# Optimization experiments

Measured on AMD Instinct MI355X. Metric: run time of the kernel, lower is better.

## Reference

```python
import jax, jax.numpy as jnp
import numpy as np

N_NODES = 50000
E_RAW = 1600000
EMB_DIM = 32
HID = 128
OUT = 128


def setup_inputs() -> dict:
    key = jax.random.key(0)
    k1, k2, k3, k4, k5, k6 = jax.random.split(key, 6)
    x = jnp.arange(N_NODES, dtype=jnp.int64)
    edge_index = jax.random.randint(k1, (2, E_RAW), 0, N_NODES, dtype=jnp.int64)
    emb = jax.random.normal(k2, (N_NODES, EMB_DIM), dtype=jnp.float32)
    W1 = jax.random.normal(k3, (EMB_DIM, HID), dtype=jnp.float32) / np.sqrt(EMB_DIM)
    b1 = jnp.zeros((HID,), dtype=jnp.float32)
    W2 = jax.random.normal(k4, (HID, OUT), dtype=jnp.float32) / np.sqrt(HID)
    b2 = jnp.zeros((OUT,), dtype=jnp.float32)
    return {"x": x, "edge_index": edge_index, "emb": emb,
            "W1": W1, "b1": b1, "W2": W2, "b2": b2}


def _gcn_norm(edge_index, num_nodes):
    # add self-loops, then symmetric normalization deg^-1/2 A_hat deg^-1/2
    loop = jnp.arange(num_nodes, dtype=edge_index.dtype)
    src = jnp.concatenate([edge_index[0], loop])
    dst = jnp.concatenate([edge_index[1], loop])
    ones = jnp.ones(src.shape[0], dtype=jnp.float32)
    deg = jax.ops.segment_sum(ones, dst, num_segments=num_nodes)
    dinv = jax.lax.rsqrt(deg)  # deg >= 1 due to self-loops
    norm = dinv[src] * dinv[dst]  # [E+N]
    return src, dst, norm


def _gcn_conv(h, src, dst, norm, W, b, num_nodes):
    h = h @ W                                  # [N, d_out] dense GEMM
    msg = h[src] * norm[:, None]               # gather + edge scale
    agg = jax.ops.segment_sum(msg, dst, num_segments=num_nodes)  # scatter-add
    return agg + b


def reference(x, edge_index, emb, W1, b1, W2, b2):
    num_nodes = emb.shape[0]
    h = emb[x]                                 # embedding lookup
    src, dst, norm = _gcn_norm(edge_index, num_nodes)
    h = _gcn_conv(h, src, dst, norm, W1, b1, num_nodes)
    h = jax.nn.relu(h)
    out = _gcn_conv(h, src, dst, norm, W2, b2, num_nodes)
    return out
```

## Files before the change

kernel.cpp:

```cpp
#include <hip/hip_runtime.h>


#define NPP   6250
#define NC    32

typedef float vfloat4 __attribute__((ext_vector_type(4)));

static inline int cdiv(int a, int b){ return (a + b - 1) / b; }

__device__ __forceinline__ unsigned short f2bf(float f){
    unsigned int u = __float_as_uint(f);
    u += 0x7fffu + ((u >> 16) & 1u);
    return (unsigned short)(u >> 16);
}
__device__ __forceinline__ float bf2f(unsigned short b){
    return __uint_as_float(((unsigned int)b) << 16);
}

__device__ __forceinline__ void nt_store4(float* p, const float4& v){
    vfloat4 t = {v.x, v.y, v.z, v.w};
    __builtin_nontemporal_store(t, (vfloat4*)p);
}

__global__ void k_zero_i32(int* __restrict__ p, int n){
    int i = blockIdx.x * blockDim.x + threadIdx.x;
    if (i < n) p[i] = 0;
}

__global__ __launch_bounds__(256) void k_bucket(const int* __restrict__ src,
        const int* __restrict__ dst, int E, int* __restrict__ staged,
        int* __restrict__ gcur, int npp, int C){
    __shared__ int qcnt[8];
    __shared__ int qbase[8];
    __shared__ int qbuf[8 * 256];
    int tid = threadIdx.x;
    if (tid < 8) qcnt[tid] = 0;
    __syncthreads();
    int e0 = blockIdx.x * 1024 + tid * 4;
    if (e0 + 3 < E){
        int4 d4 = *(const int4*)(dst + e0);
        int4 s4 = *(const int4*)(src + e0);
        int dd[4] = {d4.x, d4.y, d4.z, d4.w};
        int ss[4] = {s4.x, s4.y, s4.z, s4.w};
        #pragma unroll
        for (int i = 0; i < 4; i++){
            int p = dd[i] / npp;
            int pk = ((dd[i] - p * npp) << 17) | ss[i];
            int pos = atomicAdd(&qcnt[p], 1);
            if (pos < 256) qbuf[p * 256 + pos] = pk;
            else {
                int gp = atomicAdd(&gcur[p], 1);
                staged[(size_t)p * C + gp] = pk;
            }
        }
    } else {
        for (int e = e0; e < E && e < e0 + 4; e++){
            int d = dst[e], s = src[e];
            int p = d / npp;
            int pk = ((d - p * npp) << 17) | s;
            int pos = atomicAdd(&qcnt[p], 1);
            if (pos < 256) qbuf[p * 256 + pos] = pk;
            else {
                int gp = atomicAdd(&gcur[p], 1);
                staged[(size_t)p * C + gp] = pk;
            }
        }
    }
    __syncthreads();
    if (tid < 8){
        int nq = min(qcnt[tid], 256);
        qbase[tid] = (nq > 0) ? atomicAdd(&gcur[tid], nq) : 0;
    }
    __syncthreads();
    for (int b = 0; b < 8; b++){
        int nq = min(qcnt[b], 256);
        int gb = qbase[b];
        for (int i = tid; i < nq; i += 256)
            staged[(size_t)b * C + gb + i] = qbuf[b * 256 + i];
    }
}

__global__ __launch_bounds__(256) void k_hist(const int* __restrict__ staged,
        const int* __restrict__ gcur, int C, int CH, int npp, int* __restrict__ H){
    __shared__ int hist[NPP];
    int part  = blockIdx.x & 7;
    int chunk = blockIdx.x >> 3;
    int tid = threadIdx.x;
    for (int i = tid; i < npp; i += 256) hist[i] = 0;
    __syncthreads();
    int pc = gcur[part];
    int e0 = chunk * CH, e1 = min(e0 + CH, pc);
    const int* sd = staged + (size_t)part * C;
    for (int e = e0 + tid; e < e1; e += 256)
        atomicAdd(&hist[(unsigned)sd[e] >> 17], 1);
    __syncthreads();
    int* Hrow = H + (size_t)(part * NC + chunk) * npp;
    for (int i = tid; i < npp; i += 256) Hrow[i] = hist[i];
}

__global__ __launch_bounds__(256) void k_nodescan(int* __restrict__ H, int npp, int n,
        int* __restrict__ ecount, float* __restrict__ dinv, int* __restrict__ bsum){
    __shared__ int s[256];
    int t = blockIdx.x * 256 + threadIdx.x;
    int run = 0;
    if (t < 8 * npp && t < n){
        int p  = t / npp;
        int dl = t - p * npp;
        #pragma unroll
        for (int c = 0; c < NC; c++){
            size_t idx = (size_t)(p * NC + c) * npp + dl;
            int v = H[idx];
            H[idx] = run;
            run += v;
        }
        ecount[t] = run;
        dinv[t] = rsqrtf((float)run + 1.0f);
    }
    s[threadIdx.x] = run;
    __syncthreads();
    for (int d = 128; d > 0; d >>= 1){
        if (threadIdx.x < d) s[threadIdx.x] += s[threadIdx.x + d];
        __syncthreads();
    }
    if (threadIdx.x == 0) bsum[blockIdx.x] = s[0];
}

__global__ __launch_bounds__(256) void k_scanBC(const int* __restrict__ ecount, int n,
        const int* __restrict__ bsum, int nb, int* __restrict__ offsets){
    __shared__ int bs[256];
    __shared__ int s[256];
    int t = threadIdx.x;
    bs[t] = (t < nb) ? bsum[t] : 0;
    __syncthreads();
    if (t == 0){
        int run = 0;
        for (int b = 0; b < nb; b++){ int v = bs[b]; bs[b] = run; run += v; }
    }
    __syncthreads();
    int i = blockIdx.x * 256 + t;
    int v = (i < n) ? ecount[i] : 0;
    s[t] = v;
    __syncthreads();
    for (int d = 1; d < 256; d <<= 1){
        int x = (t >= d) ? s[t - d] : 0;
        __syncthreads();
        s[t] += x;
        __syncthreads();
    }
    if (i < n) offsets[i] = bs[blockIdx.x] + s[t] - v;
}

__global__ __launch_bounds__(256) void k_fill3(const int* __restrict__ staged,
        const int* __restrict__ gcur, int C, int CH, int npp,
        const int* __restrict__ H, const int* __restrict__ offsets,
        int* __restrict__ csr_src){
    __shared__ int cur[NPP];
    int part  = blockIdx.x & 7;
    int chunk = blockIdx.x >> 3;
    int tid = threadIdx.x;
    const int* Hrow = H + (size_t)(part * NC + chunk) * npp;
    for (int i = tid; i < npp; i += 256) cur[i] = Hrow[i];
    __syncthreads();
    int pc = gcur[part];
    int lo = part * npp;
    int e0 = chunk * CH, e1 = min(e0 + CH, pc);
    const int* sd = staged + (size_t)part * C;
    for (int e = e0 + tid; e < e1; e += 256){
        int pk = sd[e];
        int dl = (unsigned)pk >> 17;
        int r = atomicAdd(&cur[dl], 1);
        csr_src[offsets[lo + dl] + r] = pk & 0x1FFFF;
    }
}

__global__ void k_scale(const float* __restrict__ emb, const int* __restrict__ x,
                        const float* __restrict__ dinv, unsigned short* __restrict__ es, int n){
    int idx = blockIdx.x * blockDim.x + threadIdx.x;
    if (idx >= n * 32) return;
    int i = idx >> 5;
    int c = idx & 31;
    es[idx] = f2bf(emb[(size_t)x[i] * 32 + c] * dinv[i]);
}

__global__ __launch_bounds__(256) void k_l1(const unsigned short* __restrict__ es,
        const int* __restrict__ offsets, const int* __restrict__ ecount,
        const int* __restrict__ csr, const float* __restrict__ dinv,
        const float* __restrict__ W1, const float* __restrict__ b1,
        unsigned short* __restrict__ hs, int n){
    __shared__ float w[32 * 128];
    __shared__ float a1t[8][32];
    for (int i = threadIdx.x; i < 32 * 128; i += 256) w[i] = W1[i];
    int g    = threadIdx.x >> 5;
    int lane = threadIdx.x & 31;
    int node = blockIdx.x * 8 + g;
    if (node < n){
        int off = offsets[node], cnt = ecount[node];
        float s0 = bf2f(es[(size_t)node * 32 + lane]);
        float s1 = 0.f;
        int e = 0;
        for (; e + 16 <= cnt; e += 16){
            int idx[16];
            #pragma unroll
            for (int i = 0; i < 16; i++) idx[i] = csr[off + e + i];
            unsigned short v[16];
            #pragma unroll
            for (int i = 0; i < 16; i++) v[i] = es[(size_t)idx[i] * 32 + lane];
            #pragma unroll
            for (int i = 0; i < 16; i += 2){
                s0 += bf2f(v[i]);
                s1 += bf2f(v[i + 1]);
            }
        }
        for (; e + 8 <= cnt; e += 8){
            int idx[8];
            #pragma unroll
            for (int i = 0; i < 8; i++) idx[i] = csr[off + e + i];
            unsigned short v[8];
            #pragma unroll
            for (int i = 0; i < 8; i++) v[i] = es[(size_t)idx[i] * 32 + lane];
            #pragma unroll
            for (int i = 0; i < 8; i += 2){
                s0 += bf2f(v[i]);
                s1 += bf2f(v[i + 1]);
            }
        }
        for (; e < cnt; e++) s0 += bf2f(es[(size_t)csr[off + e] * 32 + lane]);
        a1t[g][lane] = dinv[node] * (s0 + s1);
    }
    __syncthreads();
    if (node >= n) return;
    int c4 = lane * 4;
    float4 acc = *(const float4*)(b1 + c4);
    #pragma unroll
    for (int k4 = 0; k4 < 8; k4++){
        float4 av = *(const float4*)&a1t[g][k4 * 4];
        float4 w0 = *(const float4*)&w[(k4 * 4 + 0) * 128 + c4];
        float4 w1 = *(const float4*)&w[(k4 * 4 + 1) * 128 + c4];
        float4 w2 = *(const float4*)&w[(k4 * 4 + 2) * 128 + c4];
        float4 w3 = *(const float4*)&w[(k4 * 4 + 3) * 128 + c4];
        acc.x += av.x * w0.x + av.y * w1.x + av.z * w2.x + av.w * w3.x;
        acc.y += av.x * w0.y + av.y * w1.y + av.z * w2.y + av.w * w3.y;
        acc.z += av.x * w0.z + av.y * w1.z + av.z * w2.z + av.w * w3.z;
        acc.w += av.x * w0.w + av.y * w1.w + av.z * w2.w + av.w * w3.w;
    }
    float dv = dinv[node];
    ushort4 o;
    o.x = f2bf(dv * fmaxf(acc.x, 0.f));
    o.y = f2bf(dv * fmaxf(acc.y, 0.f));
    o.z = f2bf(dv * fmaxf(acc.z, 0.f));
    o.w = f2bf(dv * fmaxf(acc.w, 0.f));
    *(ushort4*)(hs + (size_t)node * 128 + c4) = o;
}

__global__ __launch_bounds__(256, 5) void k_l2(const unsigned short* __restrict__ hs,
        const int* __restrict__ offsets, const int* __restrict__ ecount,
        const int* __restrict__ csr, const float* __restrict__ dinv,
        const float* __restrict__ W2, const float* __restrict__ b2,
        float* __restrict__ out, int n){
    __shared__ float a2t[32 * 128];
    int g    = threadIdx.x >> 5;
    int lane = threadIdx.x & 31;
    int c4g  = lane * 4;
    #pragma unroll
    for (int j = 0; j < 4; j++){
        int nl = g + 8 * j;
        int node = blockIdx.x * 32 + nl;
        if (node < n){
            int off = offsets[node], cnt = ecount[node];
            ushort4 sv = *(const ushort4*)(hs + (size_t)node * 128 + c4g);
            float ax0 = bf2f(sv.x), ax1 = 0.f;
            float ay0 = bf2f(sv.y), ay1 = 0.f;
            float az0 = bf2f(sv.z), az1 = 0.f;
            float aw0 = bf2f(sv.w), aw1 = 0.f;
            int e = 0;
            for (; e + 16 <= cnt; e += 16){
                int idx[16];
                #pragma unroll
                for (int i = 0; i < 16; i++) idx[i] = csr[off + e + i];
                ushort4 v[16];
                #pragma unroll
                for (int i = 0; i < 16; i++)
                    v[i] = *(const ushort4*)(hs + (size_t)idx[i] * 128 + c4g);
                #pragma unroll
                for (int i = 0; i < 16; i += 2){
                    ax0 += bf2f(v[i].x); ax1 += bf2f(v[i + 1].x);
                    ay0 += bf2f(v[i].y); ay1 += bf2f(v[i + 1].y);
                    az0 += bf2f(v[i].z); az1 += bf2f(v[i + 1].z);
                    aw0 += bf2f(v[i].w); aw1 += bf2f(v[i + 1].w);
                }
            }
            for (; e + 8 <= cnt; e += 8){
                int idx[8];
                #pragma unroll
                for (int i = 0; i < 8; i++) idx[i] = csr[off + e + i];
                ushort4 v[8];
                #pragma unroll
                for (int i = 0; i < 8; i++)
                    v[i] = *(const ushort4*)(hs + (size_t)idx[i] * 128 + c4g);
                #pragma unroll
                for (int i = 0; i < 8; i += 2){
                    ax0 += bf2f(v[i].x); ax1 += bf2f(v[i + 1].x);
                    ay0 += bf2f(v[i].y); ay1 += bf2f(v[i + 1].y);
                    az0 += bf2f(v[i].z); az1 += bf2f(v[i + 1].z);
                    aw0 += bf2f(v[i].w); aw1 += bf2f(v[i + 1].w);
                }
            }
            for (; e < cnt; e++){
                ushort4 v = *(const ushort4*)(hs + (size_t)csr[off + e] * 128 + c4g);
                ax0 += bf2f(v.x); ay0 += bf2f(v.y); az0 += bf2f(v.z); aw0 += bf2f(v.w);
            }
            float dv = dinv[node];
            float4 r;
            r.x = dv * (ax0 + ax1); r.y = dv * (ay0 + ay1);
            r.z = dv * (az0 + az1); r.w = dv * (aw0 + aw1);
            *(float4*)&a2t[nl * 128 + c4g] = r;
        }
    }
    __syncthreads();
    int c4 = lane * 4;
    int r0 = (threadIdx.x >> 5) * 4;
    float4 bias = *(const float4*)(b2 + c4);
    float4 acc0 = bias, acc1 = bias, acc2 = bias, acc3 = bias;
    for (int k = 0; k < 128; k += 4){
        float4 a0  = *(const float4*)&a2t[(r0 + 0) * 128 + k];
        float4 a1v = *(const float4*)&a2t[(r0 + 1) * 128 + k];
        float4 a2v = *(const float4*)&a2t[(r0 + 2) * 128 + k];
        float4 a3v = *(const float4*)&a2t[(r0 + 3) * 128 + k];
        #pragma unroll
        for (int kk = 0; kk < 4; kk++){
            float4 wv = *(const float4*)(W2 + (size_t)(k + kk) * 128 + c4);
            float b0 = (kk == 0) ? a0.x  : (kk == 1) ? a0.y  : (kk == 2) ? a0.z  : a0.w;
            float b1v= (kk == 0) ? a1v.x : (kk == 1) ? a1v.y : (kk == 2) ? a1v.z : a1v.w;
            float b2v= (kk == 0) ? a2v.x : (kk == 1) ? a2v.y : (kk == 2) ? a2v.z : a2v.w;
            float b3 = (kk == 0) ? a3v.x : (kk == 1) ? a3v.y : (kk == 2) ? a3v.z : a3v.w;
            acc0.x += b0 * wv.x; acc0.y += b0 * wv.y; acc0.z += b0 * wv.z; acc0.w += b0 * wv.w;
            acc1.x += b1v * wv.x; acc1.y += b1v * wv.y; acc1.z += b1v * wv.z; acc1.w += b1v * wv.w;
            acc2.x += b2v * wv.x; acc2.y += b2v * wv.y; acc2.z += b2v * wv.z; acc2.w += b2v * wv.w;
            acc3.x += b3 * wv.x; acc3.y += b3 * wv.y; acc3.z += b3 * wv.z; acc3.w += b3 * wv.w;
        }
    }
    int rb = blockIdx.x * 32 + r0;
    if (rb + 0 < n) nt_store4(out + (size_t)(rb + 0) * 128 + c4, acc0);
    if (rb + 1 < n) nt_store4(out + (size_t)(rb + 1) * 128 + c4, acc1);
    if (rb + 2 < n) nt_store4(out + (size_t)(rb + 2) * 128 + c4, acc2);
    if (rb + 3 < n) nt_store4(out + (size_t)(rb + 3) * 128 + c4, acc3);
}

extern "C" void kernel_launch(void* const* d_in, const int* in_sizes, int n_in,
                              void* d_out, int out_size, void* d_ws, size_t ws_size,
                              hipStream_t stream){
    const int*   x    = (const int*)d_in[0];
    const int*   ei   = (const int*)d_in[1];
    const float* emb  = (const float*)d_in[2];
    const float* W1   = (const float*)d_in[3];
    const float* b1   = (const float*)d_in[4];
    const float* W2   = (const float*)d_in[5];
    const float* b2   = (const float*)d_in[6];
    const int N = in_sizes[0];
    const int E = in_sizes[1] / 2;
    const int* srcv = ei;
    const int* dstv = ei + E;
    float* out = (float*)d_out;

    char* p = (char*)d_ws;
    auto alloc = [&](size_t bytes) -> char* {
        char* r = p; p += (bytes + 255) & ~(size_t)255; return r;
    };
    int nb = cdiv(N, 256);
    int*            ecount  = (int*)           alloc((size_t)(N + 8) * 4);
    int*            gcur    = ecount + N;
    int*            offsets = (int*)           alloc((size_t)N * 4);
    int*            bsum    = (int*)           alloc((size_t)nb * 4);
    float*          dinv    = (float*)         alloc((size_t)N * 4);
    int*            csr     = (int*)           alloc((size_t)E * 4);
    unsigned short* es      = (unsigned short*)alloc((size_t)N * 32 * 2);
    int*            H       = (int*)           alloc((size_t)8 * NC * NPP * 4);
    unsigned short* hs      = (unsigned short*)alloc((size_t)N * 128 * 2);
    int*            staged  = (int*)           alloc((size_t)(E + 8 * 65536) * 4);
    (void)ws_size; (void)n_in; (void)out_size;

    const int npp = cdiv(N, 8);
    const int C   = E / 8 + 65536;
    const int CH  = cdiv(C, NC);

    k_zero_i32<<<1, 64, 0, stream>>>(gcur, 8);
    k_bucket  <<<cdiv(E, 1024), 256, 0, stream>>>(srcv, dstv, E, staged, gcur, npp, C);
    k_hist    <<<8 * NC, 256, 0, stream>>>(staged, gcur, C, CH, npp, H);
    k_nodescan<<<nb, 256, 0, stream>>>(H, npp, N, ecount, dinv, bsum);
    k_scanBC  <<<nb, 256, 0, stream>>>(ecount, N, bsum, nb, offsets);
    k_fill3   <<<8 * NC, 256, 0, stream>>>(staged, gcur, C, CH, npp, H, offsets, csr);

    k_scale <<<cdiv(N * 32, 256), 256, 0, stream>>>(emb, x, dinv, es, N);
    k_l1    <<<cdiv(N, 8), 256, 0, stream>>>(es, offsets, ecount, csr, dinv, W1, b1, hs, N);

    k_l2    <<<cdiv(N, 32), 256, 0, stream>>>(hs, offsets, ecount, csr, dinv, W2, b2, out, N);
}
```

Before: 285.3 us.

## Per-wave bucket queues, 16-bit histogram, and 16-byte gathers in layer-2 aggregation

The bucketing kernel now gives each 64-thread wave its own small shared-memory queues, which spreads out LDS atomic contention, and flushes them with 8 threads per (wave, bucket) pair. The per-chunk histogram and offset table H is stored as 16-bit values, halving its traffic; this relies on per-node prefix counts fitting in 16 bits. The layer-2 gather loads 16 bytes per lane, with two half-warps each covering alternate edges and combined by a shuffle. Its tail is handled with masked loads, and the occupancy hint on launch_bounds is dropped.

```diff
diff --git a/kernel.cpp b/kernel.cpp
--- a/kernel.cpp
+++ b/kernel.cpp
@@ -30,11 +30,12 @@
 __global__ __launch_bounds__(256) void k_bucket(const int* __restrict__ src,
         const int* __restrict__ dst, int E, int* __restrict__ staged,
         int* __restrict__ gcur, int npp, int C){
-    __shared__ int qcnt[8];
-    __shared__ int qbase[8];
-    __shared__ int qbuf[8 * 256];
+    __shared__ int qcnt[4][8];
+    __shared__ int qbase[4][8];
+    __shared__ int qbuf[4][8][64];
     int tid = threadIdx.x;
-    if (tid < 8) qcnt[tid] = 0;
+    int w   = tid >> 6;
+    if ((tid & 63) < 8) qcnt[w][tid & 63] = 0;
     __syncthreads();
     int e0 = blockIdx.x * 1024 + tid * 4;
     if (e0 + 3 < E){
@@ -46,8 +47,8 @@
         for (int i = 0; i < 4; i++){
             int p = dd[i] / npp;
             int pk = ((dd[i] - p * npp) << 17) | ss[i];
-            int pos = atomicAdd(&qcnt[p], 1);
-            if (pos < 256) qbuf[p * 256 + pos] = pk;
+            int pos = atomicAdd(&qcnt[w][p], 1);
+            if (pos < 64) qbuf[w][p][pos] = pk;
             else {
                 int gp = atomicAdd(&gcur[p], 1);
                 staged[(size_t)p * C + gp] = pk;
@@ -58,8 +59,8 @@
             int d = dst[e], s = src[e];
             int p = d / npp;
             int pk = ((d - p * npp) << 17) | s;
-            int pos = atomicAdd(&qcnt[p], 1);
-            if (pos < 256) qbuf[p * 256 + pos] = pk;
+            int pos = atomicAdd(&qcnt[w][p], 1);
+            if (pos < 64) qbuf[w][p][pos] = pk;
             else {
                 int gp = atomicAdd(&gcur[p], 1);
                 staged[(size_t)p * C + gp] = pk;
@@ -67,21 +68,26 @@
         }
     }
     __syncthreads();
-    if (tid < 8){
-        int nq = min(qcnt[tid], 256);
-        qbase[tid] = (nq > 0) ? atomicAdd(&gcur[tid], nq) : 0;
-    }
-    __syncthreads();
-    for (int b = 0; b < 8; b++){
-        int nq = min(qcnt[b], 256);
-        int gb = qbase[b];
-        for (int i = tid; i < nq; i += 256)
-            staged[(size_t)b * C + gb + i] = qbuf[b * 256 + i];
+    if (tid < 32){
+        int ww = tid >> 3, b = tid & 7;
+        int nq = min(qcnt[ww][b], 64);
+        qbase[ww][b] = (nq > 0) ? atomicAdd(&gcur[b], nq) : 0;
+    }
+    __syncthreads();
+    {
+        int pair = tid >> 3;
+        int sl   = tid & 7;
+        int ww = pair >> 3, b = pair & 7;
+        int nq = min(qcnt[ww][b], 64);
+        int gb = qbase[ww][b];
+        for (int i = sl; i < nq; i += 8)
+            staged[(size_t)b * C + gb + i] = qbuf[ww][b][i];
     }
 }
 
 __global__ __launch_bounds__(256) void k_hist(const int* __restrict__ staged,
-        const int* __restrict__ gcur, int C, int CH, int npp, int* __restrict__ H){
+        const int* __restrict__ gcur, int C, int CH, int npp,
+        unsigned short* __restrict__ H){
     __shared__ int hist[NPP];
     int part  = blockIdx.x & 7;
     int chunk = blockIdx.x >> 3;
@@ -94,12 +100,13 @@
     for (int e = e0 + tid; e < e1; e += 256)
         atomicAdd(&hist[(unsigned)sd[e] >> 17], 1);
     __syncthreads();
-    int* Hrow = H + (size_t)(part * NC + chunk) * npp;
-    for (int i = tid; i < npp; i += 256) Hrow[i] = hist[i];
-}
-
-__global__ __launch_bounds__(256) void k_nodescan(int* __restrict__ H, int npp, int n,
-        int* __restrict__ ecount, float* __restrict__ dinv, int* __restrict__ bsum){
+    unsigned short* Hrow = H + (size_t)(part * NC + chunk) * npp;
+    for (int i = tid; i < npp; i += 256) Hrow[i] = (unsigned short)hist[i];
+}
+
+__global__ __launch_bounds__(256) void k_nodescan(unsigned short* __restrict__ H,
+        int npp, int n, int* __restrict__ ecount, float* __restrict__ dinv,
+        int* __restrict__ bsum){
     __shared__ int s[256];
     int t = blockIdx.x * 256 + threadIdx.x;
     int run = 0;
@@ -110,7 +117,7 @@
         for (int c = 0; c < NC; c++){
             size_t idx = (size_t)(p * NC + c) * npp + dl;
             int v = H[idx];
-            H[idx] = run;
+            H[idx] = (unsigned short)run;
             run += v;
         }
         ecount[t] = run;
@@ -152,13 +159,13 @@
 
 __global__ __launch_bounds__(256) void k_fill3(const int* __restrict__ staged,
         const int* __restrict__ gcur, int C, int CH, int npp,
-        const int* __restrict__ H, const int* __restrict__ offsets,
+        const unsigned short* __restrict__ H, const int* __restrict__ offsets,
         int* __restrict__ csr_src){
     __shared__ int cur[NPP];
     int part  = blockIdx.x & 7;
     int chunk = blockIdx.x >> 3;
     int tid = threadIdx.x;
-    const int* Hrow = H + (size_t)(part * NC + chunk) * npp;
+    const unsigned short* Hrow = H + (size_t)(part * NC + chunk) * npp;
     for (int i = tid; i < npp; i += 256) cur[i] = Hrow[i];
     __syncthreads();
     int pc = gcur[part];
@@ -252,7 +259,7 @@
     *(ushort4*)(hs + (size_t)node * 128 + c4) = o;
 }
 
-__global__ __launch_bounds__(256, 5) void k_l2(const unsigned short* __restrict__ hs,
+__global__ __launch_bounds__(256) void k_l2(const unsigned short* __restrict__ hs,
         const int* __restrict__ offsets, const int* __restrict__ ecount,
         const int* __restrict__ csr, const float* __restrict__ dinv,
         const float* __restrict__ W2, const float* __restrict__ b2,
@@ -260,60 +267,78 @@
     __shared__ float a2t[32 * 128];
     int g    = threadIdx.x >> 5;
     int lane = threadIdx.x & 31;
-    int c4g  = lane * 4;
+    int half = lane >> 4;
+    int q    = lane & 15;
     #pragma unroll
     for (int j = 0; j < 4; j++){
         int nl = g + 8 * j;
         int node = blockIdx.x * 32 + nl;
         if (node < n){
             int off = offsets[node], cnt = ecount[node];
-            ushort4 sv = *(const ushort4*)(hs + (size_t)node * 128 + c4g);
-            float ax0 = bf2f(sv.x), ax1 = 0.f;
-            float ay0 = bf2f(sv.y), ay1 = 0.f;
-            float az0 = bf2f(sv.z), az1 = 0.f;
-            float aw0 = bf2f(sv.w), aw1 = 0.f;
+            float acc[8];
+            if (half == 0){
+                uint4 sv = *(const uint4*)(hs + (size_t)node * 128 + q * 8);
+                unsigned int uu[4] = {sv.x, sv.y, sv.z, sv.w};
+                #pragma unroll
+                for (int d = 0; d < 4; d++){
+                    acc[2*d]   = __uint_as_float(uu[d] << 16);
+                    acc[2*d+1] = __uint_as_float(uu[d] & 0xFFFF0000u);
+                }
+            } else {
+                #pragma unroll
+                for (int d = 0; d < 8; d++) acc[d] = 0.f;
+            }
             int e = 0;
-            for (; e + 16 <= cnt; e += 16){
-                int idx[16];
-                #pragma unroll
-                for (int i = 0; i < 16; i++) idx[i] = csr[off + e + i];
-                ushort4 v[16];
-                #pragma unroll
-                for (int i = 0; i < 16; i++)
-                    v[i] = *(const ushort4*)(hs + (size_t)idx[i] * 128 + c4g);
-                #pragma unroll
-                for (int i = 0; i < 16; i += 2){
-                    ax0 += bf2f(v[i].x); ax1 += bf2f(v[i + 1].x);
-                    ay0 += bf2f(v[i].y); ay1 += bf2f(v[i + 1].y);
-                    az0 += bf2f(v[i].z); az1 += bf2f(v[i + 1].z);
-                    aw0 += bf2f(v[i].w); aw1 += bf2f(v[i + 1].w);
+            for (; e + 8 <= cnt; e += 8){
+                int id[4];
+                #pragma unroll
+                for (int i = 0; i < 4; i++) id[i] = csr[off + e + 2*i + half];
+                uint4 v[4];
+                #pragma unroll
+                for (int i = 0; i < 4; i++)
+                    v[i] = *(const uint4*)(hs + (size_t)id[i] * 128 + q * 8);
+                #pragma unroll
+                for (int i = 0; i < 4; i++){
+                    unsigned int uu[4] = {v[i].x, v[i].y, v[i].z, v[i].w};
+                    #pragma unroll
+                    for (int d = 0; d < 4; d++){
+                        acc[2*d]   += __uint_as_float(uu[d] << 16);
+                        acc[2*d+1] += __uint_as_float(uu[d] & 0xFFFF0000u);
+                    }
                 }
             }
-            for (; e + 8 <= cnt; e += 8){
-                int idx[8];
-                #pragma unroll
-                for (int i = 0; i < 8; i++) idx[i] = csr[off + e + i];
-                ushort4 v[8];
-                #pragma unroll
-                for (int i = 0; i < 8; i++)
-                    v[i] = *(const ushort4*)(hs + (size_t)idx[i] * 128 + c4g);
-                #pragma unroll
-                for (int i = 0; i < 8; i += 2){
-                    ax0 += bf2f(v[i].x); ax1 += bf2f(v[i + 1].x);
-                    ay0 += bf2f(v[i].y); ay1 += bf2f(v[i + 1].y);
-                    az0 += bf2f(v[i].z); az1 += bf2f(v[i + 1].z);
-                    aw0 += bf2f(v[i].w); aw1 += bf2f(v[i + 1].w);
+            if (e < cnt){
+                int id[4]; float m[4];
+                #pragma unroll
+                for (int i = 0; i < 4; i++){
+                    int ei = e + 2*i + half;
+                    m[i]  = (ei < cnt) ? 1.f : 0.f;
+                    id[i] = csr[off + min(ei, cnt - 1)];
                 }
-            }
-            for (; e < cnt; e++){
-                ushort4 v = *(const ushort4*)(hs + (size_t)csr[off + e] * 128 + c4g);
-                ax0 += bf2f(v.x); ay0 += bf2f(v.y); az0 += bf2f(v.z); aw0 += bf2f(v.w);
+                uint4 v[4];
+                #pragma unroll
+                for (int i = 0; i < 4; i++)
+                    v[i] = *(const uint4*)(hs + (size_t)id[i] * 128 + q * 8);
+                #pragma unroll
+                for (int i = 0; i < 4; i++){
+                    unsigned int uu[4] = {v[i].x, v[i].y, v[i].z, v[i].w};
+                    #pragma unroll
+                    for (int d = 0; d < 4; d++){
+                        acc[2*d]   += m[i] * __uint_as_float(uu[d] << 16);
+                        acc[2*d+1] += m[i] * __uint_as_float(uu[d] & 0xFFFF0000u);
+                    }
+                }
             }
             float dv = dinv[node];
-            float4 r;
-            r.x = dv * (ax0 + ax1); r.y = dv * (ay0 + ay1);
-            r.z = dv * (az0 + az1); r.w = dv * (aw0 + aw1);
-            *(float4*)&a2t[nl * 128 + c4g] = r;
+            #pragma unroll
+            for (int d = 0; d < 8; d++)
+                acc[d] += __shfl_xor(acc[d], 16, 32);
+            if (half == 0){
+                float4 r0 = {dv*acc[0], dv*acc[1], dv*acc[2], dv*acc[3]};
+                float4 r1 = {dv*acc[4], dv*acc[5], dv*acc[6], dv*acc[7]};
+                *(float4*)&a2t[nl * 128 + q * 8]     = r0;
+                *(float4*)&a2t[nl * 128 + q * 8 + 4] = r1;
+            }
         }
     }
     __syncthreads();
@@ -374,7 +399,7 @@
     float*          dinv    = (float*)         alloc((size_t)N * 4);
     int*            csr     = (int*)           alloc((size_t)E * 4);
     unsigned short* es      = (unsigned short*)alloc((size_t)N * 32 * 2);
-    int*            H       = (int*)           alloc((size_t)8 * NC * NPP * 4);
+    unsigned short* H       = (unsigned short*)alloc((size_t)8 * NC * NPP * 2);
     unsigned short* hs      = (unsigned short*)alloc((size_t)N * 128 * 2);
     int*            staged  = (int*)           alloc((size_t)(E + 8 * 65536) * 4);
     (void)ws_size; (void)n_in; (void)out_size;
```

Measured after the change: 341.6 us. 1.2x slower.
